# Optimization experiments

Hardware: AMD Instinct MI355X
Metric: run time of the kernel (lower is better)

## Reference

```python
import jax, jax.numpy as jnp
import numpy as np
import math

B, NIN, DIM, QK, GS, L, BINS = 512, 128, 512, 128, 32, 2, 100
HID = int(DIM * 2.0)
G = NIN // GS
ROT = 32  # rotary dim = min(32, query_key_dim)
EPS = 1e-5


def setup_inputs() -> dict:
    key = jax.random.key(0)
    ks = jax.random.split(key, 8)
    r = jax.random.normal
    return {
        "tokens": jax.random.randint(ks[0], (B, NIN), 0, BINS),
        "emb": r(ks[1], (NIN, BINS, DIM), jnp.float32) * 0.02,
        "pos_emb": r(ks[2], (NIN, DIM), jnp.float32) * 0.01,
        "norm_g": jnp.ones((L,), jnp.float32),
        "Wh": r(ks[3], (L, DIM, 2 * HID), jnp.float32) / math.sqrt(DIM),
        "bh": jnp.zeros((L, 2 * HID), jnp.float32),
        "Wqk": r(ks[4], (L, DIM, QK), jnp.float32) / math.sqrt(DIM),
        "bqk": jnp.zeros((L, QK), jnp.float32),
        "gamma": r(ks[5], (L, 4, QK), jnp.float32) * 0.02,
        "beta": jnp.zeros((L, 4, QK), jnp.float32),
        "rp": r(ks[6], (L, 32), jnp.float32) * 0.02,
        "Wout": r(ks[7], (L, HID, DIM), jnp.float32) / math.sqrt(HID),
        "bout": jnp.zeros((L, DIM), jnp.float32),
        "ln_g": jnp.ones((DIM,), jnp.float32),
        "ln_b": jnp.zeros((DIM,), jnp.float32),
    }


def _t5_buckets(n, num_buckets=32, max_distance=128):
    # causal T5 relative position buckets, computed statically
    pos = np.arange(n)
    rel = pos[None, :] - pos[:, None]
    neg = np.maximum(-rel, 0)
    max_exact = num_buckets // 2
    vl = max_exact + (np.log(np.maximum(neg, 1) / max_exact) / np.log(max_distance / max_exact) * (num_buckets - max_exact)).astype(np.int64)
    vl = np.minimum(vl, num_buckets - 1)
    return jnp.asarray(np.where(neg < max_exact, neg, vl))


def _rotary_cos_sin(n):
    inv = 1.0 / (10000.0 ** (np.arange(0, ROT, 2) / ROT))
    f = np.einsum('i,j->ij', np.arange(n), inv)  # [n, ROT/2]
    f = np.repeat(f, 2, axis=-1)                 # interleaved-pair freqs [n, ROT]
    return jnp.asarray(np.cos(f), jnp.float32), jnp.asarray(np.sin(f), jnp.float32)


def _apply_rotary(x, cos, sin):
    xr, xp = x[..., :ROT], x[..., ROT:]
    x2 = xr.reshape(*xr.shape[:-1], ROT // 2, 2)
    rh = jnp.stack((-x2[..., 1], x2[..., 0]), axis=-1).reshape(xr.shape)
    return jnp.concatenate([xr * cos + rh * sin, xp], axis=-1)


def reference(tokens, emb, pos_emb, norm_g, Wh, bh, Wqk, bqk, gamma, beta, rp, Wout, bout, ln_g, ln_b):
    # per-column embedding lookup + positional embedding
    x = emb[jnp.arange(NIN)[None, :], tokens] + pos_emb  # [B, NIN, DIM]
    buckets = _t5_buckets(GS)
    cos, sin = _rotary_cos_sin(NIN)
    t5_scale = QK ** 0.5
    causal_mask = jnp.triu(jnp.ones((GS, GS), bool), 1)

    def grp(t):
        return t.reshape(B, G, GS, t.shape[-1])

    def layer(h, p):
        ng, Wh_l, bh_l, Wqk_l, bqk_l, gm, bt, rp_l, Wo_l, bo_l = p
        # ScaleNorm
        nrm = jnp.linalg.norm(h, axis=-1, keepdims=True) * DIM ** -0.5
        nx = h / jnp.maximum(nrm, EPS) * ng
        # shift_tokens: shift first half of features by one position
        xs, xp = nx[..., :DIM // 2], nx[..., DIM // 2:]
        xs = jnp.pad(xs, ((0, 0), (1, 0), (0, 0)))[:, :-1]
        nx = jnp.concatenate([xs, xp], axis=-1)
        hid = jax.nn.silu(nx @ Wh_l + bh_l)
        v, gate = hid[..., :HID], hid[..., HID:]
        qk = jax.nn.silu(nx @ Wqk_l + bqk_l)
        qs = qk[..., None, :] * gm + bt  # [B, NIN, 4, QK]
        quad_q = _apply_rotary(qs[..., 0, :], cos, sin)
        lin_q = _apply_rotary(qs[..., 1, :], cos, sin)
        quad_k = _apply_rotary(qs[..., 2, :], cos, sin)
        lin_k = _apply_rotary(qs[..., 3, :], cos, sin)
        qq, lq, kk, lk, vg = map(grp, (quad_q, lin_q, quad_k, lin_k, v))
        # grouped quadratic attention with ReLU^2 attn fn and T5 rel-pos bias
        sim = jnp.einsum('bgid,bgjd->bgij', qq, kk) / GS + rp_l[buckets] * t5_scale
        attn = jnp.square(jax.nn.relu(sim))
        attn = jnp.where(causal_mask, 0.0, attn)
        quad_out = jnp.einsum('bgij,bgje->bgie', attn, vg)
        # causal linear attention across groups (shifted cumsum of kv stats)
        lin_kv = jnp.einsum('bgnd,bgne->bgde', lk, vg) / GS
        lin_kv = jnp.cumsum(lin_kv, axis=1)
        lin_kv = jnp.pad(lin_kv, ((0, 0), (1, 0), (0, 0), (0, 0)))[:, :-1]
        lin_out = jnp.einsum('bgde,bgnd->bgne', lin_kv, lq)
        out = gate * (quad_out + lin_out).reshape(B, NIN, HID)
        return out @ Wo_l + bo_l + h, None

    x, _ = jax.lax.scan(layer, x, (norm_g, Wh, bh, Wqk, bqk, gamma, beta, rp, Wout, bout))
    mu = x.mean(-1, keepdims=True)
    var = x.var(-1, keepdims=True)
    return (x - mu) / jnp.sqrt(var + EPS) * ln_g + ln_b
```

## Files before the change

kernel.cpp:

```cpp
#include <hip/hip_runtime.h>
#include <hip/hip_bf16.h>
#include <math.h>
#include <stdint.h>

#define BB   512
#define NIN  128
#define DIMD 512
#define QKD  128
#define GSZ  32
#define GRP  4
#define HID  1024
#define HID2 2048
#define NFUSE 2176
#define ROT  32
#define NLAYER 2
#define EPSF 1e-5f
#define BINS 100

typedef __bf16 bf16x8 __attribute__((ext_vector_type(8)));
typedef float  f32x4  __attribute__((ext_vector_type(4)));
typedef float  f32x16 __attribute__((ext_vector_type(16)));

__device__ __forceinline__ unsigned short f2bf(float f) {
    union { float f; uint32_t u; } v; v.f = f;
    return (unsigned short)((v.u + 0x7FFFu + ((v.u >> 16) & 1u)) >> 16);
}
__device__ __forceinline__ float bf2f(unsigned short h) {
    union { uint32_t u; float f; } v; v.u = ((uint32_t)h) << 16;
    return v.f;
}

__global__ void k_embed(const int* __restrict__ tokens, const float* __restrict__ emb,
                        const float* __restrict__ pos, float* __restrict__ h) {
    int bn = blockIdx.x;
    int n  = bn % NIN;
    int tok = tokens[bn];
    const float4* e4 = (const float4*)(emb + ((size_t)n * BINS + tok) * DIMD);
    const float4* p4 = (const float4*)(pos + (size_t)n * DIMD);
    float4* h4 = (float4*)(h + (size_t)bn * DIMD);
    int t = threadIdx.x;
    float4 a = e4[t], b = p4[t];
    h4[t] = make_float4(a.x + b.x, a.y + b.y, a.z + b.z, a.w + b.w);
}

__global__ void k_rms(const float* __restrict__ h, float* __restrict__ scale,
                      const float* __restrict__ ngp) {
    int row  = blockIdx.x * 4 + (threadIdx.x >> 6);
    int lane = threadIdx.x & 63;
    const float4* r4 = (const float4*)(h + (size_t)row * DIMD);
    float s = 0.f;
    #pragma unroll
    for (int i = 0; i < 2; ++i) {
        float4 v = r4[lane + 64 * i];
        s += v.x * v.x + v.y * v.y + v.z * v.z + v.w * v.w;
    }
    #pragma unroll
    for (int o = 32; o; o >>= 1) s += __shfl_down(s, o);
    if (lane == 0) {
        float nrm = sqrtf(s) * (1.0f / sqrtf((float)DIMD));
        scale[row] = ngp[0] / fmaxf(nrm, EPSF);
    }
}

__global__ void k_nx(const float* __restrict__ h, const float* __restrict__ scale,
                     unsigned short* __restrict__ nx) {
    int bn = blockIdx.x; int n = bn % NIN;
    int t = threadIdx.x;
    float4 v; float sc;
    if (t < 64) {
        if (n == 0) {
            ((ushort4*)(nx + (size_t)bn * DIMD))[t] = make_ushort4(0, 0, 0, 0);
            return;
        }
        sc = scale[bn - 1];
        v = ((const float4*)(h + (size_t)(bn - 1) * DIMD))[t];
    } else {
        sc = scale[bn];
        v = ((const float4*)(h + (size_t)bn * DIMD))[t];
    }
    ushort4 o = make_ushort4(f2bf(v.x * sc), f2bf(v.y * sc), f2bf(v.z * sc), f2bf(v.w * sc));
    ((ushort4*)(nx + (size_t)bn * DIMD))[t] = o;
}

__global__ void k_wcast(const float* __restrict__ W, unsigned short* __restrict__ Wt,
                        int K, int N) {
    int idx = blockIdx.x * 256 + threadIdx.x;
    int total = N * (K / 8);
    if (idx >= total) return;
    int kb = idx / N, n = idx % N;
    #pragma unroll
    for (int j = 0; j < 8; ++j)
        Wt[(size_t)n * K + kb * 8 + j] = f2bf(W[(size_t)(kb * 8 + j) * N + n]);
}

#define GLOAD_LDS(gp, lp) __builtin_amdgcn_global_load_lds( \
    (const __attribute__((address_space(1))) uint32_t*)(gp), \
    (__attribute__((address_space(3))) uint32_t*)(lp), 16, 0, 0)

template<int MODE>
__global__ __launch_bounds__(256) void k_gemm_bf16(
        const unsigned short* __restrict__ A,
        const unsigned short* __restrict__ Bt,
        const float* __restrict__ bias0,
        const float* __restrict__ bias1,
        const float* __restrict__ resid,
        float* __restrict__ Cf,
        unsigned short* __restrict__ vTp,
        unsigned short* __restrict__ gatep,
        int M, int N, int K) {
    __shared__ unsigned short As[128 * 32];
    __shared__ unsigned short Bs[128 * 32];
    const int tid  = threadIdx.x;

    int flat = blockIdx.y * gridDim.x + blockIdx.x;
    int nwg  = gridDim.x * gridDim.y;
    int q = nwg >> 3, r = nwg & 7;
    int xcd = flat & 7, idx = flat >> 3;
    int swz = (xcd < r ? xcd * (q + 1) : r * (q + 1) + (xcd - r) * q) + idx;
    const int bxi = swz % gridDim.x, byi = swz / gridDim.x;
    const int bm = byi * 128, bn = bxi * 128;

    const int lane = tid & 63, wave = tid >> 6;
    const int wm = (wave >> 1) * 64, wn = (wave & 1) * 64;
    const int l15 = lane & 15, l4 = lane >> 4;

    f32x4 acc[4][4];
    #pragma unroll
    for (int i = 0; i < 4; ++i)
        #pragma unroll
        for (int j = 0; j < 4; ++j) acc[i][j] = (f32x4){0.f, 0.f, 0.f, 0.f};

    const int rowA = tid >> 2;
    const int colB = (tid & 3) * 16;
    const char* gA = (const char*)(A  + (size_t)(bm + rowA) * K) + colB;
    const char* gB = (const char*)(Bt + (size_t)(bn + rowA) * K) + colB;
    const size_t stride64 = (size_t)64 * K * 2;
    unsigned short* ldsA = As + tid * 8;
    unsigned short* ldsB = Bs + tid * 8;

    for (int k0 = 0; k0 < K; k0 += 32) {
        GLOAD_LDS(gA + (size_t)k0 * 2,            ldsA);
        GLOAD_LDS(gA + (size_t)k0 * 2 + stride64, ldsA + 2048);
        GLOAD_LDS(gB + (size_t)k0 * 2,            ldsB);
        GLOAD_LDS(gB + (size_t)k0 * 2 + stride64, ldsB + 2048);
        asm volatile("s_waitcnt vmcnt(0)" ::: "memory");
        __syncthreads();

        bf16x8 af[4], bfr[4];
        #pragma unroll
        for (int f = 0; f < 4; ++f) {
            af[f]  = *(const bf16x8*)&As[(wm + f * 16 + l15) * 32 + l4 * 8];
            bfr[f] = *(const bf16x8*)&Bs[(wn + f * 16 + l15) * 32 + l4 * 8];
        }
        #pragma unroll
        for (int i = 0; i < 4; ++i)
            #pragma unroll
            for (int j = 0; j < 4; ++j)
                acc[i][j] = __builtin_amdgcn_mfma_f32_16x16x32_bf16(af[i], bfr[j], acc[i][j], 0, 0, 0);
        __syncthreads();
    }

    #pragma unroll
    for (int i = 0; i < 4; ++i) {
        const int n0 = wm + i * 16 + l4 * 4;
        #pragma unroll
        for (int j = 0; j < 4; ++j) {
            const int col = bn + wn + j * 16 + l15;
            if (MODE == 0) {
                float bsv = (col < 2 * HID) ? bias0[col] : bias1[col - 2 * HID];
                float vv[4];
                #pragma unroll
                for (int rr = 0; rr < 4; ++rr) {
                    float v = acc[i][j][rr] + bsv;
                    vv[rr] = v / (1.0f + __expf(-v));
                }
                if (col < HID) {
                    ushort4 o = make_ushort4(f2bf(vv[0]), f2bf(vv[1]), f2bf(vv[2]), f2bf(vv[3]));
                    *(ushort4*)&vTp[((size_t)byi * HID + col) * NIN + n0] = o;
                } else if (col < 2 * HID) {
                    #pragma unroll
                    for (int rr = 0; rr < 4; ++rr)
                        gatep[(size_t)(bm + n0 + rr) * HID + (col - HID)] = f2bf(vv[rr]);
                } else {
                    #pragma unroll
                    for (int rr = 0; rr < 4; ++rr)
                        Cf[(size_t)(bm + n0 + rr) * QKD + (col - 2 * HID)] = vv[rr];
                }
            } else {
                float bsv = bias0[col];
                #pragma unroll
                for (int rr = 0; rr < 4; ++rr) {
                    size_t row = bm + n0 + rr;
                    Cf[row * N + col] = acc[i][j][rr] + bsv + resid[row * N + col];
                }
            }
        }
    }
}

__global__ void k_cossin(float* __restrict__ cosb, float* __restrict__ sinb) {
    int idx = blockIdx.x * 256 + threadIdx.x;
    if (idx >= NIN * 16) return;
    int n = idx / 16, i = idx % 16;
    double inv = pow(10000.0, -(double)(2 * i) / (double)ROT);
    double f = (double)n * inv;
    cosb[idx] = (float)cos(f);
    sinb[idx] = (float)sin(f);
}

__global__ void k_rot(const float* __restrict__ qk, const float* __restrict__ gm,
                      const float* __restrict__ bt, const float* __restrict__ cosb,
                      const float* __restrict__ sinb, unsigned short* __restrict__ q4) {
    int bn = blockIdx.x; int n = bn % NIN;
    int d = threadIdx.x;
    float x = qk[(size_t)bn * QKD + d];
    float xp0 = 0.f;
    int dp = d ^ 1;
    if (d < ROT) xp0 = qk[(size_t)bn * QKD + dp];
    #pragma unroll
    for (int c = 0; c < 4; ++c) {
        float val = x * gm[c * QKD + d] + bt[c * QKD + d];
        float outv;
        if (d < ROT) {
            int i = d >> 1;
            float cs = cosb[n * 16 + i], sn = sinb[n * 16 + i];
            float xp = xp0 * gm[c * QKD + dp] + bt[c * QKD + dp];
            outv = ((d & 1) == 0) ? (val * cs - xp * sn) : (val * cs + xp * sn);
        } else outv = val;
        q4[((size_t)bn * 4 + c) * QKD + d] = f2bf(outv);
    }
}

__global__ __launch_bounds__(256) void k_attn2(
        const unsigned short* __restrict__ q4,
        const unsigned short* __restrict__ gatep,
        const unsigned short* __restrict__ vT,
        const float* __restrict__ rp,
        unsigned short* __restrict__ attn_out) {
    int et = blockIdx.x, b = blockIdx.y;
    int tid = threadIdx.x, wave = tid >> 6, lane = tid & 63;
    int l31 = lane & 31, lhi = lane >> 5;

    __shared__ unsigned short S[32][136];
    __shared__ float rps_d[32];
    if (tid < 32) {
        int d = tid, bucket;
        if (d < 16) bucket = d;
        else {
            bucket = 16 + (int)(logf((float)d * (1.0f / 16.0f)) * (16.0f / logf(8.0f)));
            if (bucket > 31) bucket = 31;
        }
        rps_d[tid] = rp[bucket] * sqrtf((float)QKD);
    }
    __syncthreads();

    size_t bbase = (size_t)b * NIN;
    int e0 = et * 256 + wave * 64;
    const unsigned short* vbase = vT + (size_t)b * HID * NIN;

    for (int g = 0; g < GRP; ++g) {
        if (wave <= g) {
            int gp = wave;
            bool quad = (gp == g);
            const unsigned short* Qb = q4 + ((bbase + g  * 32 + l31) * 4 + (quad ? 0 : 1)) * QKD;
            const unsigned short* Kb = q4 + ((bbase + gp * 32 + l31) * 4 + (quad ? 2 : 3)) * QKD;
            f32x16 sa = {};
            #pragma unroll
            for (int kk = 0; kk < 8; ++kk) {
                bf16x8 aq = *(const bf16x8*)(Qb + kk * 16 + lhi * 8);
                bf16x8 bk = *(const bf16x8*)(Kb + kk * 16 + lhi * 8);
                sa = __builtin_amdgcn_mfma_f32_32x32x16_bf16(aq, bk, sa, 0, 0, 0);
            }
            int j = l31;
            #pragma unroll
            for (int r = 0; r < 16; ++r) {
                int i = (r & 3) + 8 * (r >> 2) + 4 * lhi;
                float s = sa[r] * (1.0f / GSZ);
                if (quad) {
                    if (j > i) s = 0.f;
                    else {
                        s += rps_d[i - j];
                        s = fmaxf(s, 0.f);
                        s = s * s;
                    }
                }
                S[i][gp * 32 + j] = f2bf(s);
            }
        }
        __syncthreads();

        f32x16 o0 = {}, o1 = {};
        int KT = 2 * (g + 1);
        for (int kk = 0; kk < KT; ++kk) {
            int k0 = kk * 16 + lhi * 8;
            bf16x8 af = *(const bf16x8*)&S[l31][k0];
            bf16x8 b0 = *(const bf16x8*)(vbase + (size_t)(e0 + l31) * NIN + k0);
            bf16x8 b1 = *(const bf16x8*)(vbase + (size_t)(e0 + 32 + l31) * NIN + k0);
            o0 = __builtin_amdgcn_mfma_f32_32x32x16_bf16(af, b0, o0, 0, 0, 0);
            o1 = __builtin_amdgcn_mfma_f32_32x32x16_bf16(af, b1, o1, 0, 0, 0);
        }
        __syncthreads();

        int ea = e0 + l31, eb = e0 + 32 + l31;
        #pragma unroll
        for (int r = 0; r < 16; ++r) {
            int i = (r & 3) + 8 * (r >> 2) + 4 * lhi;
            size_t row = bbase + g * 32 + i;
            float ga = bf2f(gatep[row * HID + ea]);
            float gb = bf2f(gatep[row * HID + eb]);
            attn_out[row * HID + ea] = f2bf(ga * o0[r]);
            attn_out[row * HID + eb] = f2bf(gb * o1[r]);
        }
    }
}

__global__ void k_ln(const float* __restrict__ h, const float* __restrict__ lng,
                     const float* __restrict__ lnb, float* __restrict__ out) {
    int bn = blockIdx.x;
    int t = threadIdx.x;
    const float4* r4 = (const float4*)(h + (size_t)bn * DIMD);
    float4 v = r4[t];
    float s  = v.x + v.y + v.z + v.w;
    float sq = v.x * v.x + v.y * v.y + v.z * v.z + v.w * v.w;
    __shared__ float red[4];
    #pragma unroll
    for (int o = 32; o; o >>= 1) { s += __shfl_down(s, o); sq += __shfl_down(sq, o); }
    int lane = t & 63, w = t >> 6;
    if (lane == 0) { red[w] = s; red[2 + w] = sq; }
    __syncthreads();
    float mu  = (red[0] + red[1]) * (1.0f / DIMD);
    float var = (red[2] + red[3]) * (1.0f / DIMD) - mu * mu;
    float rstd = 1.0f / sqrtf(var + EPSF);
    float4 gg = ((const float4*)lng)[t];
    float4 bb = ((const float4*)lnb)[t];
    float4 o;
    o.x = (v.x - mu) * rstd * gg.x + bb.x;
    o.y = (v.y - mu) * rstd * gg.y + bb.y;
    o.z = (v.z - mu) * rstd * gg.z + bb.z;
    o.w = (v.w - mu) * rstd * gg.w + bb.w;
    ((float4*)(out + (size_t)bn * DIMD))[t] = o;
}

extern "C" void kernel_launch(void* const* d_in, const int* in_sizes, int n_in,
                              void* d_out, int out_size, void* d_ws, size_t ws_size,
                              hipStream_t stream) {
    const int*   tokens = (const int*)d_in[0];
    const float* emb    = (const float*)d_in[1];
    const float* pos    = (const float*)d_in[2];
    const float* norm_g = (const float*)d_in[3];
    const float* Wh     = (const float*)d_in[4];
    const float* bh     = (const float*)d_in[5];
    const float* Wqk    = (const float*)d_in[6];
    const float* bqk    = (const float*)d_in[7];
    const float* gamma  = (const float*)d_in[8];
    const float* beta   = (const float*)d_in[9];
    const float* rp     = (const float*)d_in[10];
    const float* Wout   = (const float*)d_in[11];
    const float* bout   = (const float*)d_in[12];
    const float* lng    = (const float*)d_in[13];
    const float* lnb    = (const float*)d_in[14];

    float* h  = (float*)d_out;
    float* ws = (float*)d_ws;

    size_t off = 0;
    float* scale = ws + off; off += (size_t)BB * NIN;
    float* cosb  = ws + off; off += NIN * 16;
    float* sinb  = ws + off; off += NIN * 16;
    unsigned short* whqkT = (unsigned short*)(ws + off); off += (size_t)NLAYER * NFUSE * DIMD / 2;
    unsigned short* woutT = (unsigned short*)(ws + off); off += (size_t)NLAYER * DIMD * HID / 2;
    off = (off + 63) & ~(size_t)63;
    const size_t fixedFloats = off;

    const size_t wsFloats = ws_size / sizeof(float);
    const size_t perBatch = (size_t)NIN * (DIMD / 2 + HID / 2 + HID / 2 + QKD + DIMD / 2 + HID / 2);
    int CB = BB;
    while (CB > 1 && fixedFloats + (size_t)CB * perBatch + 64 > wsFloats) CB >>= 1;

    unsigned short* nx    = (unsigned short*)(ws + off); off += (size_t)CB * NIN * DIMD / 2;
    unsigned short* vT    = (unsigned short*)(ws + off); off += (size_t)CB * HID * NIN / 2;
    unsigned short* gateB = (unsigned short*)(ws + off); off += (size_t)CB * NIN * HID / 2;
    float*          qk    = ws + off;                    off += (size_t)CB * NIN * QKD;
    unsigned short* q4    = (unsigned short*)(ws + off); off += (size_t)CB * NIN * DIMD / 2;
    unsigned short* attnB = (unsigned short*)(ws + off); off += (size_t)CB * NIN * HID / 2;

    const int BN_ = BB * NIN;

    k_cossin<<<8, 256, 0, stream>>>(cosb, sinb);
    k_embed<<<BN_, 128, 0, stream>>>(tokens, emb, pos, h);

    for (int l = 0; l < NLAYER; ++l) {
        unsigned short* whqkT_l = whqkT + (size_t)l * NFUSE * DIMD;
        k_wcast<<<(HID2 * DIMD / 8 + 255) / 256, 256, 0, stream>>>(
            Wh + (size_t)l * DIMD * HID2,  whqkT_l, DIMD, HID2);
        k_wcast<<<(QKD * DIMD / 8 + 255) / 256, 256, 0, stream>>>(
            Wqk + (size_t)l * DIMD * QKD,  whqkT_l + (size_t)HID2 * DIMD, DIMD, QKD);
        k_wcast<<<(DIMD * HID / 8 + 255) / 256, 256, 0, stream>>>(
            Wout + (size_t)l * HID * DIMD, woutT + (size_t)l * DIMD * HID, HID, DIMD);
    }

    for (int l = 0; l < NLAYER; ++l) {
        const float* bh_l  = bh   + (size_t)l * HID2;
        const float* bqk_l = bqk  + (size_t)l * QKD;
        const float* gm_l  = gamma+ (size_t)l * 4 * QKD;
        const float* bt_l  = beta + (size_t)l * 4 * QKD;
        const float* rp_l  = rp   + (size_t)l * 32;
        const float* bo_l  = bout + (size_t)l * DIMD;
        const unsigned short* whqkT_l = whqkT + (size_t)l * NFUSE * DIMD;
        const unsigned short* woutT_l = woutT + (size_t)l * DIMD * HID;

        for (int c0 = 0; c0 < BB; c0 += CB) {
            const int rowsC = CB * NIN;
            float* h_c = h + (size_t)c0 * NIN * DIMD;

            k_rms<<<rowsC / 4, 256, 0, stream>>>(h_c, scale, norm_g + l);
            k_nx<<<rowsC, 128, 0, stream>>>(h_c, scale, nx);

            dim3 g1(NFUSE / 128, rowsC / 128);
            k_gemm_bf16<0><<<g1, 256, 0, stream>>>(nx, whqkT_l, bh_l, bqk_l, nullptr,
                                                   qk, vT, gateB, rowsC, NFUSE, DIMD);

            k_rot<<<rowsC, 128, 0, stream>>>(qk, gm_l, bt_l, cosb, sinb, q4);

            dim3 ga(HID / 256, CB);
            k_attn2<<<ga, 256, 0, stream>>>(q4, gateB, vT, rp_l, attnB);

            dim3 g3(DIMD / 128, rowsC / 128);
            k_gemm_bf16<1><<<g3, 256, 0, stream>>>(attnB, woutT_l, bo_l, nullptr, h_c,
                                                   h_c, nullptr, nullptr, rowsC, DIMD, HID);
        }
    }

    k_ln<<<BN_, 128, 0, stream>>>(h, lng, lnb, (float*)d_out);
}
```

Before: 1.523 ms.

## Enlarge GEMM tile to 256x128 with double-buffered LDS and XOR swizzle

Reworks the bf16 MFMA GEMM to use a 256x128 block tile, where each wave owns a 64x128 sub-tile. LDS is double-buffered so the next K-slice is loaded while the current one is multiplied. An XOR swizzle on the LDS column layout reduces bank conflicts. This raises arithmetic intensity per loaded byte, overlaps global loads with MFMA work, and removes one barrier per iteration. In exchange it doubles accumulator registers (128 floats per thread), uses 48KB of LDS, and halves the number of workgroups, which can lower occupancy.

After: 1.429 ms. 1.07x faster.

```diff
diff --git a/kernel.cpp b/kernel.cpp
--- a/kernel.cpp
+++ b/kernel.cpp
@@ -98,7 +98,7 @@
     (__attribute__((address_space(3))) uint32_t*)(lp), 16, 0, 0)
 
 template<int MODE>
-__global__ __launch_bounds__(256) void k_gemm_bf16(
+__global__ __launch_bounds__(256, 2) void k_gemm2(
         const unsigned short* __restrict__ A,
         const unsigned short* __restrict__ Bt,
         const float* __restrict__ bias0,
@@ -108,9 +108,9 @@
         unsigned short* __restrict__ vTp,
         unsigned short* __restrict__ gatep,
         int M, int N, int K) {
-    __shared__ unsigned short As[128 * 32];
-    __shared__ unsigned short Bs[128 * 32];
-    const int tid  = threadIdx.x;
+    __shared__ unsigned short As[2][256 * 32];
+    __shared__ unsigned short Bs[2][128 * 32];
+    const int tid = threadIdx.x;
 
     int flat = blockIdx.y * gridDim.x + blockIdx.x;
     int nwg  = gridDim.x * gridDim.y;
@@ -118,65 +118,92 @@
     int xcd = flat & 7, idx = flat >> 3;
     int swz = (xcd < r ? xcd * (q + 1) : r * (q + 1) + (xcd - r) * q) + idx;
     const int bxi = swz % gridDim.x, byi = swz / gridDim.x;
-    const int bm = byi * 128, bn = bxi * 128;
+    const int bm = byi * 256, bn = bxi * 128;
 
     const int lane = tid & 63, wave = tid >> 6;
-    const int wm = (wave >> 1) * 64, wn = (wave & 1) * 64;
     const int l15 = lane & 15, l4 = lane >> 4;
 
-    f32x4 acc[4][4];
+    f32x4 acc[4][8];
     #pragma unroll
     for (int i = 0; i < 4; ++i)
         #pragma unroll
-        for (int j = 0; j < 4; ++j) acc[i][j] = (f32x4){0.f, 0.f, 0.f, 0.f};
+        for (int j = 0; j < 8; ++j) acc[i][j] = (f32x4){0.f, 0.f, 0.f, 0.f};
 
     const int rowA = tid >> 2;
-    const int colB = (tid & 3) * 16;
-    const char* gA = (const char*)(A  + (size_t)(bm + rowA) * K) + colB;
-    const char* gB = (const char*)(Bt + (size_t)(bn + rowA) * K) + colB;
+    const int colO = (tid & 3) * 16;
+    const int colS = colO ^ ((rowA & 3) << 4);
+    const char* gA = (const char*)(A  + (size_t)(bm + rowA) * K) + colS;
+    const char* gB = (const char*)(Bt + (size_t)(bn + rowA) * K) + colS;
     const size_t stride64 = (size_t)64 * K * 2;
-    unsigned short* ldsA = As + tid * 8;
-    unsigned short* ldsB = Bs + tid * 8;
-
-    for (int k0 = 0; k0 < K; k0 += 32) {
-        GLOAD_LDS(gA + (size_t)k0 * 2,            ldsA);
-        GLOAD_LDS(gA + (size_t)k0 * 2 + stride64, ldsA + 2048);
-        GLOAD_LDS(gB + (size_t)k0 * 2,            ldsB);
-        GLOAD_LDS(gB + (size_t)k0 * 2 + stride64, ldsB + 2048);
+    unsigned short* dA0 = &As[0][tid * 8];
+    unsigned short* dA1 = &As[1][tid * 8];
+    unsigned short* dB0 = &Bs[0][tid * 8];
+    unsigned short* dB1 = &Bs[1][tid * 8];
+
+    #define STAGE2(dA, dB, k0) do { \
+        const char* sA_ = gA + (size_t)(k0) * 2; \
+        const char* sB_ = gB + (size_t)(k0) * 2; \
+        GLOAD_LDS(sA_,                 (dA)); \
+        GLOAD_LDS(sA_ +     stride64,  (dA) + 2048); \
+        GLOAD_LDS(sA_ + 2 * stride64,  (dA) + 4096); \
+        GLOAD_LDS(sA_ + 3 * stride64,  (dA) + 6144); \
+        GLOAD_LDS(sB_,                 (dB)); \
+        GLOAD_LDS(sB_ +     stride64,  (dB) + 2048); \
+    } while (0)
+
+    STAGE2(dA0, dB0, 0);
+    asm volatile("s_waitcnt vmcnt(0)" ::: "memory");
+    __syncthreads();
+
+    const int NIT = K / 32;
+    int bufc = 0;
+    for (int it = 0; it < NIT; ++it) {
+        if (it + 1 < NIT) {
+            if (bufc == 0) STAGE2(dA1, dB1, (it + 1) * 32);
+            else           STAGE2(dA0, dB0, (it + 1) * 32);
+        }
+        const unsigned short* Ab = As[bufc];
+        const unsigned short* Bb = Bs[bufc];
+        bf16x8 af[4], bfr[8];
+        #pragma unroll
+        for (int f = 0; f < 4; ++f) {
+            int rA = wave * 64 + f * 16 + l15;
+            af[f] = *(const bf16x8*)&Ab[rA * 32 + ((l4 ^ (rA & 3)) << 3)];
+        }
+        #pragma unroll
+        for (int c = 0; c < 8; ++c) {
+            int rB = c * 16 + l15;
+            bfr[c] = *(const bf16x8*)&Bb[rB * 32 + ((l4 ^ (rB & 3)) << 3)];
+        }
+        #pragma unroll
+        for (int f = 0; f < 4; ++f)
+            #pragma unroll
+            for (int c = 0; c < 8; ++c)
+                acc[f][c] = __builtin_amdgcn_mfma_f32_16x16x32_bf16(af[f], bfr[c], acc[f][c], 0, 0, 0);
         asm volatile("s_waitcnt vmcnt(0)" ::: "memory");
         __syncthreads();
-
-        bf16x8 af[4], bfr[4];
-        #pragma unroll
-        for (int f = 0; f < 4; ++f) {
-            af[f]  = *(const bf16x8*)&As[(wm + f * 16 + l15) * 32 + l4 * 8];
-            bfr[f] = *(const bf16x8*)&Bs[(wn + f * 16 + l15) * 32 + l4 * 8];
-        }
-        #pragma unroll
-        for (int i = 0; i < 4; ++i)
-            #pragma unroll
-            for (int j = 0; j < 4; ++j)
-                acc[i][j] = __builtin_amdgcn_mfma_f32_16x16x32_bf16(af[i], bfr[j], acc[i][j], 0, 0, 0);
-        __syncthreads();
-    }
-
-    #pragma unroll
-    for (int i = 0; i < 4; ++i) {
-        const int n0 = wm + i * 16 + l4 * 4;
-        #pragma unroll
-        for (int j = 0; j < 4; ++j) {
-            const int col = bn + wn + j * 16 + l15;
+        bufc ^= 1;
+    }
+    #undef STAGE2
+
+    #pragma unroll
+    for (int f = 0; f < 4; ++f) {
+        const int n0 = wave * 64 + f * 16 + l4 * 4;
+        #pragma unroll
+        for (int c = 0; c < 8; ++c) {
+            const int col = bn + c * 16 + l15;
             if (MODE == 0) {
                 float bsv = (col < 2 * HID) ? bias0[col] : bias1[col - 2 * HID];
                 float vv[4];
                 #pragma unroll
                 for (int rr = 0; rr < 4; ++rr) {
-                    float v = acc[i][j][rr] + bsv;
+                    float v = acc[f][c][rr] + bsv;
                     vv[rr] = v / (1.0f + __expf(-v));
                 }
                 if (col < HID) {
+                    size_t batch = (size_t)byi * 2 + (n0 >> 7);
                     ushort4 o = make_ushort4(f2bf(vv[0]), f2bf(vv[1]), f2bf(vv[2]), f2bf(vv[3]));
-                    *(ushort4*)&vTp[((size_t)byi * HID + col) * NIN + n0] = o;
+                    *(ushort4*)&vTp[(batch * HID + col) * NIN + (n0 & 127)] = o;
                 } else if (col < 2 * HID) {
                     #pragma unroll
                     for (int rr = 0; rr < 4; ++rr)
@@ -191,7 +218,7 @@
                 #pragma unroll
                 for (int rr = 0; rr < 4; ++rr) {
                     size_t row = bm + n0 + rr;
-                    Cf[row * N + col] = acc[i][j][rr] + bsv + resid[row * N + col];
+                    Cf[row * N + col] = acc[f][c][rr] + bsv + resid[row * N + col];
                 }
             }
         }
@@ -375,7 +402,7 @@
     const size_t wsFloats = ws_size / sizeof(float);
     const size_t perBatch = (size_t)NIN * (DIMD / 2 + HID / 2 + HID / 2 + QKD + DIMD / 2 + HID / 2);
     int CB = BB;
-    while (CB > 1 && fixedFloats + (size_t)CB * perBatch + 64 > wsFloats) CB >>= 1;
+    while (CB > 2 && fixedFloats + (size_t)CB * perBatch + 64 > wsFloats) CB >>= 1;
 
     unsigned short* nx    = (unsigned short*)(ws + off); off += (size_t)CB * NIN * DIMD / 2;
     unsigned short* vT    = (unsigned short*)(ws + off); off += (size_t)CB * HID * NIN / 2;
@@ -416,18 +443,18 @@
             k_rms<<<rowsC / 4, 256, 0, stream>>>(h_c, scale, norm_g + l);
             k_nx<<<rowsC, 128, 0, stream>>>(h_c, scale, nx);
 
-            dim3 g1(NFUSE / 128, rowsC / 128);
-            k_gemm_bf16<0><<<g1, 256, 0, stream>>>(nx, whqkT_l, bh_l, bqk_l, nullptr,
-                                                   qk, vT, gateB, rowsC, NFUSE, DIMD);
+            dim3 g1(NFUSE / 128, rowsC / 256);
+            k_gemm2<0><<<g1, 256, 0, stream>>>(nx, whqkT_l, bh_l, bqk_l, nullptr,
+                                               qk, vT, gateB, rowsC, NFUSE, DIMD);
 
             k_rot<<<rowsC, 128, 0, stream>>>(qk, gm_l, bt_l, cosb, sinb, q4);
 
             dim3 ga(HID / 256, CB);
             k_attn2<<<ga, 256, 0, stream>>>(q4, gateB, vT, rp_l, attnB);
 
-            dim3 g3(DIMD / 128, rowsC / 128);
-            k_gemm_bf16<1><<<g3, 256, 0, stream>>>(attnB, woutT_l, bo_l, nullptr, h_c,
-                                                   h_c, nullptr, nullptr, rowsC, DIMD, HID);
+            dim3 g3(DIMD / 128, rowsC / 256);
+            k_gemm2<1><<<g3, 256, 0, stream>>>(attnB, woutT_l, bo_l, nullptr, h_c,
+                                               h_c, nullptr, nullptr, rowsC, DIMD, HID);
         }
     }
 
```
